# Kernel optimization log

Hardware: AMD Instinct MI355X
Metric: run time of the kernel (lower is better)

The kernel has to match this reference:

```python
import jax, jax.numpy as jnp
import numpy as np

ROPE_THETA = 10000.0
NUM_HEADS = 16


def apply_rope(x, pos, theta=ROPE_THETA):
    # x: [b, h, s, d_h]; pos: [s] int positions
    d = x.shape[-1]
    inv_freq = 1.0 / (theta ** (jnp.arange(0, d, 2, dtype=jnp.float32) / d))  # [d/2]
    ang = pos.astype(jnp.float32)[:, None] * inv_freq[None, :]  # [s, d/2]
    cos, sin = jnp.cos(ang), jnp.sin(ang)
    x1, x2 = x[..., 0::2], x[..., 1::2]  # interleaved pairs
    r1 = x1 * cos - x2 * sin
    r2 = x1 * sin + x2 * cos
    return jnp.stack([r1, r2], axis=-1).reshape(x.shape)


def setup_inputs() -> dict:
    key = jax.random.key(0)
    k1, k2, k3 = jax.random.split(key, 3)
    B, S, D = 4, 2048, 1024
    x = jax.random.normal(k1, (B, S, D), dtype=jnp.float32)
    W_qkv = jax.random.normal(k2, (3, D, D), dtype=jnp.float32) * 0.02
    W_o = jax.random.normal(k3, (D, D), dtype=jnp.float32) * 0.02
    token_positions = jnp.arange(S, dtype=jnp.int32)
    return {"x": x, "W_qkv": W_qkv, "W_o": W_o, "token_positions": token_positions}


def reference(x, W_qkv, W_o, token_positions):
    B, S, D = x.shape
    H = NUM_HEADS
    dh = D // H
    # fused QKV projection: [3, b, s, d]
    qkv = jnp.einsum('bsd,kod->kbso', x, W_qkv)
    # split heads: [3, b, h, s, d_h]
    qkv = qkv.reshape(3, B, S, H, dh).transpose(0, 1, 3, 2, 4)
    q, k, v = qkv[0], qkv[1], qkv[2]
    q = apply_rope(q, token_positions)
    k = apply_rope(k, token_positions)
    scores = jnp.einsum('bhqd,bhkd->bhqk', q, k) / jnp.sqrt(jnp.float32(dh))
    causal = jnp.tril(jnp.ones((S, S), dtype=bool))
    scores = jnp.where(causal, scores, jnp.finfo(scores.dtype).min)
    probs = jax.nn.softmax(scores, axis=-1)
    out = jnp.einsum('bhqk,bhkd->bhqd', probs, v)
    out = out.transpose(0, 2, 1, 3).reshape(B, S, D)  # merge heads
    return out @ W_o.T
```

## Files before the change

### kernel.cpp

```cpp
#include <hip/hip_runtime.h>

typedef unsigned short ushort_t;
typedef unsigned int uint_t;
typedef __bf16 bf16_t;
typedef bf16_t bf16x8 __attribute__((ext_vector_type(8)));
typedef float floatx4 __attribute__((ext_vector_type(4)));

typedef const __attribute__((address_space(1))) uint_t* gptr_t;
typedef __attribute__((address_space(3))) uint_t* lptr_t;

#define BATCH 4
#define SEQ   2048
#define DMODEL 1024
#define NHEAD 16
#define DH    64
#define BHSD  (BATCH*NHEAD*SEQ*DH)
#define QSCALE 0.18033688f
#define MFIX2  11.5415603f

#define NX4 (BATCH*SEQ*DMODEL/4)
#define NW4 (3*DMODEL*DMODEL/4)
#define NO4 (DMODEL*DMODEL/4)
#define NTB (SEQ*32)
#define NSETUP (NX4+NW4+NO4+NTB)

__device__ __forceinline__ float b2f(ushort_t u) {
    uint_t x = ((uint_t)u) << 16;
    return __uint_as_float(x);
}
__device__ __forceinline__ ushort_t f2b(float f) {
    uint_t u = __float_as_uint(f);
    u = (u + 0x7fffu + ((u >> 16) & 1u)) >> 16;
    return (ushort_t)u;
}

__global__ __launch_bounds__(256) void setup_kernel(
    const float* __restrict__ x_f, const float* __restrict__ wq_f,
    const float* __restrict__ wo_f, const int* __restrict__ tp,
    ushort_t* __restrict__ xb, ushort_t* __restrict__ wqb,
    ushort_t* __restrict__ wob, float* __restrict__ ct,
    float* __restrict__ st)
{
    int idx = blockIdx.x * 256 + threadIdx.x;
    if (idx < NX4) {
        float4 v = *(const float4*)&x_f[idx * 4];
        ushort4 o;
        o.x = f2b(v.x); o.y = f2b(v.y); o.z = f2b(v.z); o.w = f2b(v.w);
        *(ushort4*)&xb[idx * 4] = o;
    } else if (idx < NX4 + NW4) {
        int i = idx - NX4;
        float4 v = *(const float4*)&wq_f[i * 4];
        ushort4 o;
        o.x = f2b(v.x); o.y = f2b(v.y); o.z = f2b(v.z); o.w = f2b(v.w);
        *(ushort4*)&wqb[i * 4] = o;
    } else if (idx < NX4 + NW4 + NO4) {
        int i = idx - (NX4 + NW4);
        float4 v = *(const float4*)&wo_f[i * 4];
        ushort4 o;
        o.x = f2b(v.x); o.y = f2b(v.y); o.z = f2b(v.z); o.w = f2b(v.w);
        *(ushort4*)&wob[i * 4] = o;
    } else {
        int i = idx - (NX4 + NW4 + NO4);
        int s = i >> 5;
        int fi = i & 31;
        float pos = (float)tp[s];
        float invf = expf(-(float)fi * 0.28782313662425572f);
        float sv, cv;
        sincosf(pos * invf, &sv, &cv);
        ct[i] = cv;
        st[i] = sv;
    }
}

__device__ __forceinline__ void gemm_bt_tile(
    const ushort_t* __restrict__ A, const ushort_t* __restrict__ B, int K,
    int mbase, int nbase, floatx4 acc[4][4],
    ushort_t* __restrict__ As, ushort_t* __restrict__ Bs)
{
    const int tid  = threadIdx.x;
    const int lane = tid & 63;
    const int wave = tid >> 6;
    const int wm   = (wave >> 1) << 6;
    const int wn   = (wave & 1) << 6;
    const int quad = lane >> 4;
    const int l16  = lane & 15;
    const int lrow = lane >> 3;
    const int lcol = (((lane & 7) ^ lrow) << 3);
    const int rsw  = l16 & 7;

#pragma unroll
    for (int mi = 0; mi < 4; mi++)
#pragma unroll
        for (int ni = 0; ni < 4; ni++)
            acc[mi][ni] = (floatx4){0.f, 0.f, 0.f, 0.f};

    for (int k0 = 0; k0 < K; k0 += 64) {
        __syncthreads();
#pragma unroll
        for (int c = 0; c < 4; ++c) {
            int chunk = wave * 4 + c;
            int row = chunk * 8 + lrow;
            __builtin_amdgcn_global_load_lds(
                (gptr_t)&A[(size_t)(mbase + row) * K + k0 + lcol],
                (lptr_t)&As[chunk * 512], 16, 0, 0);
            __builtin_amdgcn_global_load_lds(
                (gptr_t)&B[(size_t)(nbase + row) * K + k0 + lcol],
                (lptr_t)&Bs[chunk * 512], 16, 0, 0);
        }
        __syncthreads();

#pragma unroll
        for (int kq = 0; kq < 2; ++kq) {
            const int cg = ((kq * 4 + quad) ^ rsw) * 8;
            bf16x8 af[4], bfr[4];
#pragma unroll
            for (int i = 0; i < 4; i++)
                af[i]  = *(const bf16x8*)&As[(wm + i * 16 + l16) * 64 + cg];
#pragma unroll
            for (int i = 0; i < 4; i++)
                bfr[i] = *(const bf16x8*)&Bs[(wn + i * 16 + l16) * 64 + cg];

#pragma unroll
            for (int mi = 0; mi < 4; mi++)
#pragma unroll
                for (int ni = 0; ni < 4; ni++)
                    acc[mi][ni] = __builtin_amdgcn_mfma_f32_16x16x32_bf16(
                        af[mi], bfr[ni], acc[mi][ni], 0, 0, 0);
        }
    }
}

__global__ __launch_bounds__(256) void qkv_rope_kernel(
    const ushort_t* __restrict__ x, const ushort_t* __restrict__ Wqkv,
    const float* __restrict__ ctab, const float* __restrict__ stab,
    ushort_t* __restrict__ qkv)
{
    __shared__ __align__(16) ushort_t As[128 * 64];
    __shared__ __align__(16) ushort_t Bs[128 * 64];
    __shared__ __align__(16) ushort_t T[32 * 136];
    floatx4 acc[4][4];

    const int which = blockIdx.z;
    const int mbase = blockIdx.x * 128;
    const int nbase = blockIdx.y * 128;

    gemm_bt_tile(x, Wqkv + (size_t)which * DMODEL * DMODEL, DMODEL,
                 mbase, nbase, acc, As, Bs);

    const int tid  = threadIdx.x;
    const int lane = tid & 63;
    const int wave = tid >> 6;
    const int wm = (wave >> 1) << 6, wn = (wave & 1) << 6;
    const int quad = lane >> 4, l16 = lane & 15;
    const int wrow0 = (wm ? 16 : 0) + quad * 4;

    for (int mi = 0; mi < 4; mi++) {
#pragma unroll
        for (int ni = 0; ni < 4; ni++) {
#pragma unroll
            for (int r = 0; r < 4; r++) {
                int grow = mbase + wm + mi * 16 + quad * 4 + r;
                int gcol = nbase + wn + ni * 16 + l16;
                float val = acc[mi][ni][r];
                float partner = __shfl_xor(val, 1);
                int s  = grow & (SEQ - 1);
                int dd = gcol & (DH - 1);
                float res = val;
                if (which < 2) {
                    int fi = dd >> 1;
                    float cs = ctab[s * 32 + fi];
                    float sn = stab[s * 32 + fi];
                    res = (gcol & 1) ? fmaf(partner, sn, val * cs)
                                     : fmaf(val, cs, -partner * sn);
                }
                if (which == 0) res *= QSCALE;
                T[(wrow0 + r) * 136 + wn + ni * 16 + l16] = f2b(res);
            }
        }
        __syncthreads();

#pragma unroll
        for (int cc = 0; cc < 2; ++cc) {
            int c = cc * 256 + tid;
            int q2 = c >> 7, ci = c & 127;
            int rgrp = q2 >> 1, hh = q2 & 1;
            int growb = mbase + rgrp * 64;
            int bb = growb >> 11;
            int hidx = (nbase >> 6) + hh;
            size_t bufb = ((size_t)bb * NHEAD + hidx) * ((size_t)SEQ * DH);
            if (which == 0) {
                int row16 = ci >> 3, dd8 = (ci & 7) << 3;
                int s = (growb & (SEQ - 1)) + mi * 16 + row16;
                uint4 d = *(const uint4*)&T[(rgrp * 16 + row16) * 136 + hh * 64 + dd8];
                *(uint4*)&qkv[bufb + (size_t)s * DH + dd8] = d;
            } else {
                int kt = (growb & (SEQ - 1)) >> 6;
                if (which == 1) {
                    int kc = ci >> 6, rem = ci & 63;
                    int qd = rem >> 4, lk = rem & 15;
                    int cflat = (kc * 4 + mi) * 64 + qd * 16 + lk;
                    uint4 d = *(const uint4*)&T[(rgrp * 16 + lk) * 136 + hh * 64 + kc * 32 + qd * 8];
                    *(uint4*)&qkv[(size_t)BHSD + bufb + (size_t)kt * 4096 + cflat * 8] = d;
                } else {
                    int tt = ci >> 6, rem = ci & 63;
                    int nd = rem >> 4, lv = rem & 15;
                    int cflat = ((mi >> 1) * 4 + nd) * 64 + ((mi * 2 + tt) & 3) * 16 + lv;
                    ushort_t tmp[8];
#pragma unroll
                    for (int j = 0; j < 8; ++j)
                        tmp[j] = T[(rgrp * 16 + tt * 8 + j) * 136 + hh * 64 + nd * 16 + lv];
                    *(uint4*)&qkv[2 * (size_t)BHSD + bufb + (size_t)kt * 4096 + cflat * 8]
                        = *(uint4*)tmp;
                }
            }
        }
        __syncthreads();
    }
}

__global__ __launch_bounds__(64) void attn_mfma_kernel(
    const ushort_t* __restrict__ q, const ushort_t* __restrict__ kf,
    const ushort_t* __restrict__ vf, ushort_t* __restrict__ attnout)
{
    __shared__ __align__(16) ushort_t Pw[32 * 72];

    const int lane = threadIdx.x;
    const int quad = lane >> 4;
    const int l16  = lane & 15;
    const int bid = blockIdx.x;
    const int bh = (bid & 7) * 8 + ((bid >> 3) & 7);
    const int chunk = 63 - (bid >> 6);
    const int b = bh >> 4, h = bh & 15;
    const size_t base = (size_t)bh * SEQ * DH;
    const int q0w = chunk * 32;

    bf16x8 qf[2][2];
#pragma unroll
    for (int mi = 0; mi < 2; mi++)
#pragma unroll
        for (int kc = 0; kc < 2; kc++)
            qf[mi][kc] = *(const bf16x8*)&q[base
                + (size_t)(q0w + mi * 16 + l16) * DH + kc * 32 + quad * 8];

    floatx4 o[2][4];
    float lp[2][4];
#pragma unroll
    for (int mi = 0; mi < 2; mi++)
#pragma unroll
        for (int nd = 0; nd < 4; nd++)
            o[mi][nd] = (floatx4){0.f, 0.f, 0.f, 0.f};
#pragma unroll
    for (int mi = 0; mi < 2; mi++)
#pragma unroll
        for (int r = 0; r < 4; r++)
            lp[mi][r] = 0.f;

    const int ktmax = (q0w + 31) >> 6;

    for (int kt = 0; kt <= ktmax; ++kt) {
        const ushort_t* ktb = &kf[base + (size_t)kt * 4096];
        const ushort_t* vtb = &vf[base + (size_t)kt * 4096];

        floatx4 s[2][4];
#pragma unroll
        for (int mi = 0; mi < 2; mi++)
#pragma unroll
            for (int ni = 0; ni < 4; ni++)
                s[mi][ni] = (floatx4){0.f, 0.f, 0.f, 0.f};
#pragma unroll
        for (int kc = 0; kc < 2; kc++) {
            bf16x8 kfr[4];
#pragma unroll
            for (int ni = 0; ni < 4; ni++)
                kfr[ni] = *(const bf16x8*)&ktb[(kc * 4 + ni) * 512 + lane * 8];
#pragma unroll
            for (int mi = 0; mi < 2; mi++)
#pragma unroll
                for (int ni = 0; ni < 4; ni++)
                    s[mi][ni] = __builtin_amdgcn_mfma_f32_16x16x32_bf16(
                        qf[mi][kc], kfr[ni], s[mi][ni], 0, 0, 0);
        }

        bf16x8 vfr[2][4];
#pragma unroll
        for (int kc = 0; kc < 2; kc++)
#pragma unroll
            for (int nd = 0; nd < 4; nd++)
                vfr[kc][nd] = *(const bf16x8*)&vtb[(kc * 4 + nd) * 512 + lane * 8];

        const bool needs_mask = (kt == ktmax);

#pragma unroll
        for (int mi = 0; mi < 2; mi++) {
#pragma unroll
            for (int r = 0; r < 4; r++) {
                if (needs_mask) {
                    int row_g = q0w + mi * 16 + quad * 4 + r;
#pragma unroll
                    for (int ni = 0; ni < 4; ni++) {
                        int col_g = kt * 64 + ni * 16 + l16;
                        s[mi][ni][r] = (col_g <= row_g) ? s[mi][ni][r]
                                                        : -INFINITY;
                    }
                }
                float acc = 0.f;
#pragma unroll
                for (int ni = 0; ni < 4; ni++) {
                    float p = exp2f(s[mi][ni][r] - MFIX2);
                    s[mi][ni][r] = p;
                    acc += p;
                }
                lp[mi][r] += acc;
            }
        }

#pragma unroll
        for (int mi = 0; mi < 2; mi++)
#pragma unroll
            for (int ni = 0; ni < 4; ni++)
#pragma unroll
                for (int r = 0; r < 4; r++)
                    Pw[(mi * 16 + quad * 4 + r) * 72 + ni * 16 + l16]
                        = f2b(s[mi][ni][r]);

#pragma unroll
        for (int kc = 0; kc < 2; kc++) {
            bf16x8 pf[2];
#pragma unroll
            for (int mi = 0; mi < 2; mi++)
                pf[mi] = *(const bf16x8*)&Pw[(mi * 16 + l16) * 72 + kc * 32 + quad * 8];
#pragma unroll
            for (int mi = 0; mi < 2; mi++)
#pragma unroll
                for (int nd = 0; nd < 4; nd++)
                    o[mi][nd] = __builtin_amdgcn_mfma_f32_16x16x32_bf16(
                        pf[mi], vfr[kc][nd], o[mi][nd], 0, 0, 0);
        }
    }

#pragma unroll
    for (int mi = 0; mi < 2; mi++)
#pragma unroll
        for (int r = 0; r < 4; r++) {
            float lf = lp[mi][r];
            lf += __shfl_xor(lf, 1);
            lf += __shfl_xor(lf, 2);
            lf += __shfl_xor(lf, 4);
            lf += __shfl_xor(lf, 8);
            lp[mi][r] = 1.0f / lf;
        }
#pragma unroll
    for (int mi = 0; mi < 2; mi++)
#pragma unroll
        for (int nd = 0; nd < 4; nd++)
#pragma unroll
            for (int r = 0; r < 4; r++) {
                int s_idx = q0w + mi * 16 + quad * 4 + r;
                float val = o[mi][nd][r] * lp[mi][r];
                attnout[((size_t)(b * SEQ + s_idx)) * DMODEL + h * DH + nd * 16 + l16]
                    = f2b(val);
            }
}

__global__ __launch_bounds__(256) void outproj_kernel(
    const ushort_t* __restrict__ Ain, const ushort_t* __restrict__ Wo,
    float* __restrict__ out)
{
    __shared__ __align__(16) ushort_t As[128 * 64];
    __shared__ __align__(16) ushort_t Bs[128 * 64];
    floatx4 acc[4][4];

    const int mbase = blockIdx.x * 128;
    const int nbase = blockIdx.y * 128;
    gemm_bt_tile(Ain, Wo, DMODEL, mbase, nbase, acc, As, Bs);

    const int lane = threadIdx.x & 63;
    const int wave = threadIdx.x >> 6;
    const int wm = (wave >> 1) << 6, wn = (wave & 1) << 6;
    const int quad = lane >> 4, l16 = lane & 15;

#pragma unroll
    for (int mi = 0; mi < 4; mi++)
#pragma unroll
        for (int ni = 0; ni < 4; ni++)
#pragma unroll
            for (int r = 0; r < 4; r++) {
                int grow = mbase + wm + mi * 16 + quad * 4 + r;
                int gcol = nbase + wn + ni * 16 + l16;
                out[(size_t)grow * DMODEL + gcol] = acc[mi][ni][r];
            }
}

extern "C" void kernel_launch(void* const* d_in, const int* in_sizes, int n_in,
                              void* d_out, int out_size, void* d_ws, size_t ws_size,
                              hipStream_t stream) {
    const float* x_f    = (const float*)d_in[0];
    const float* Wqkv_f = (const float*)d_in[1];
    const float* Wo_f   = (const float*)d_in[2];
    const int* tp       = (const int*)d_in[3];
    float* out          = (float*)d_out;

    char* ws = (char*)d_ws;
    ushort_t* qkv     = (ushort_t*)(ws);
    ushort_t* attnout = (ushort_t*)(ws + 50331648);
    float* ctab       = (float*)(ws + 67108864);
    float* stab       = (float*)(ws + 67371008);
    ushort_t* xb      = (ushort_t*)(ws + 67633152);
    ushort_t* Wqkvb   = (ushort_t*)(ws + 84410368);
    ushort_t* Wob     = (ushort_t*)(ws + 90701824);

    setup_kernel<<<dim3(NSETUP / 256), dim3(256), 0, stream>>>(
        x_f, Wqkv_f, Wo_f, tp, xb, Wqkvb, Wob, ctab, stab);

    qkv_rope_kernel<<<dim3(BATCH * SEQ / 128, DMODEL / 128, 3), dim3(256), 0, stream>>>(
        xb, Wqkvb, ctab, stab, qkv);

    attn_mfma_kernel<<<dim3(4096), dim3(64), 0, stream>>>(
        qkv, qkv + (size_t)BHSD, qkv + 2 * (size_t)BHSD, attnout);

    outproj_kernel<<<dim3(BATCH * SEQ / 128, DMODEL / 128), dim3(256), 0, stream>>>(
        attnout, Wob, out);
}
```

Baseline: 280.7 us.

## Process 64 query rows per attention wave to reuse K/V tiles

```diff
diff --git a/kernel.cpp b/kernel.cpp
--- a/kernel.cpp
+++ b/kernel.cpp
@@ -222,64 +222,49 @@
     const ushort_t* __restrict__ q, const ushort_t* __restrict__ kf,
     const ushort_t* __restrict__ vf, ushort_t* __restrict__ attnout)
 {
-    __shared__ __align__(16) ushort_t Pw[32 * 72];
+    __shared__ __align__(16) ushort_t Pw[64 * 72];
 
     const int lane = threadIdx.x;
     const int quad = lane >> 4;
     const int l16  = lane & 15;
     const int bid = blockIdx.x;
     const int bh = (bid & 7) * 8 + ((bid >> 3) & 7);
-    const int chunk = 63 - (bid >> 6);
+    const int g  = 31 - (bid >> 6);
     const int b = bh >> 4, h = bh & 15;
     const size_t base = (size_t)bh * SEQ * DH;
-    const int q0w = chunk * 32;
-
-    bf16x8 qf[2][2];
-#pragma unroll
-    for (int mi = 0; mi < 2; mi++)
+    const int q0w = g * 64;
+
+    bf16x8 qf[4][2];
+#pragma unroll
+    for (int mi = 0; mi < 4; mi++)
 #pragma unroll
         for (int kc = 0; kc < 2; kc++)
             qf[mi][kc] = *(const bf16x8*)&q[base
                 + (size_t)(q0w + mi * 16 + l16) * DH + kc * 32 + quad * 8];
 
-    floatx4 o[2][4];
-    float lp[2][4];
-#pragma unroll
-    for (int mi = 0; mi < 2; mi++)
+    floatx4 o[4][4];
+    float lp[4][4];
+#pragma unroll
+    for (int mi = 0; mi < 4; mi++)
 #pragma unroll
         for (int nd = 0; nd < 4; nd++)
             o[mi][nd] = (floatx4){0.f, 0.f, 0.f, 0.f};
 #pragma unroll
-    for (int mi = 0; mi < 2; mi++)
+    for (int mi = 0; mi < 4; mi++)
 #pragma unroll
         for (int r = 0; r < 4; r++)
             lp[mi][r] = 0.f;
 
-    const int ktmax = (q0w + 31) >> 6;
-
-    for (int kt = 0; kt <= ktmax; ++kt) {
+    for (int kt = 0; kt <= g; ++kt) {
         const ushort_t* ktb = &kf[base + (size_t)kt * 4096];
         const ushort_t* vtb = &vf[base + (size_t)kt * 4096];
 
-        floatx4 s[2][4];
-#pragma unroll
-        for (int mi = 0; mi < 2; mi++)
+        bf16x8 kfr[2][4];
+#pragma unroll
+        for (int kc = 0; kc < 2; kc++)
 #pragma unroll
             for (int ni = 0; ni < 4; ni++)
-                s[mi][ni] = (floatx4){0.f, 0.f, 0.f, 0.f};
-#pragma unroll
-        for (int kc = 0; kc < 2; kc++) {
-            bf16x8 kfr[4];
-#pragma unroll
-            for (int ni = 0; ni < 4; ni++)
-                kfr[ni] = *(const bf16x8*)&ktb[(kc * 4 + ni) * 512 + lane * 8];
-#pragma unroll
-            for (int mi = 0; mi < 2; mi++)
-#pragma unroll
-                for (int ni = 0; ni < 4; ni++)
-                    s[mi][ni] = __builtin_amdgcn_mfma_f32_16x16x32_bf16(
-                        qf[mi][kc], kfr[ni], s[mi][ni], 0, 0, 0);
-        }
+                kfr[kc][ni] = *(const bf16x8*)&ktb[(kc * 4 + ni) * 512 + lane * 8];
 
         bf16x8 vfr[2][4];
 #pragma unroll
@@ -288,49 +273,67 @@
             for (int nd = 0; nd < 4; nd++)
                 vfr[kc][nd] = *(const bf16x8*)&vtb[(kc * 4 + nd) * 512 + lane * 8];
 
-        const bool needs_mask = (kt == ktmax);
-
-#pragma unroll
-        for (int mi = 0; mi < 2; mi++) {
-#pragma unroll
-            for (int r = 0; r < 4; r++) {
-                if (needs_mask) {
-                    int row_g = q0w + mi * 16 + quad * 4 + r;
+        const bool needs_mask = (kt == g);
+
+#pragma unroll
+        for (int hh = 0; hh < 2; ++hh) {
+            floatx4 s[2][4];
+#pragma unroll
+            for (int m2 = 0; m2 < 2; m2++)
+#pragma unroll
+                for (int ni = 0; ni < 4; ni++)
+                    s[m2][ni] = (floatx4){0.f, 0.f, 0.f, 0.f};
+#pragma unroll
+            for (int kc = 0; kc < 2; kc++)
+#pragma unroll
+                for (int m2 = 0; m2 < 2; m2++)
+#pragma unroll
+                    for (int ni = 0; ni < 4; ni++)
+                        s[m2][ni] = __builtin_amdgcn_mfma_f32_16x16x32_bf16(
+                            qf[hh * 2 + m2][kc], kfr[kc][ni], s[m2][ni], 0, 0, 0);
+
+#pragma unroll
+            for (int m2 = 0; m2 < 2; m2++) {
+#pragma unroll
+                for (int r = 0; r < 4; r++) {
+                    if (needs_mask) {
+                        int row_g = q0w + (hh * 2 + m2) * 16 + quad * 4 + r;
+#pragma unroll
+                        for (int ni = 0; ni < 4; ni++) {
+                            int col_g = q0w + ni * 16 + l16;
+                            s[m2][ni][r] = (col_g <= row_g) ? s[m2][ni][r]
+                                                            : -INFINITY;
+                        }
+                    }
+                    float accv = 0.f;
 #pragma unroll
                     for (int ni = 0; ni < 4; ni++) {
-                        int col_g = kt * 64 + ni * 16 + l16;
-                        s[mi][ni][r] = (col_g <= row_g) ? s[mi][ni][r]
-                                                        : -INFINITY;
+                        float p = exp2f(s[m2][ni][r] - MFIX2);
+                        s[m2][ni][r] = p;
+                        accv += p;
                     }
+                    lp[hh * 2 + m2][r] += accv;
                 }
-                float acc = 0.f;
-#pragma unroll
-                for (int ni = 0; ni < 4; ni++) {
-                    float p = exp2f(s[mi][ni][r] - MFIX2);
-                    s[mi][ni][r] = p;
-                    acc += p;
-                }
-                lp[mi][r] += acc;
             }
-        }
-
-#pragma unroll
-        for (int mi = 0; mi < 2; mi++)
-#pragma unroll
-            for (int ni = 0; ni < 4; ni++)
-#pragma unroll
-                for (int r = 0; r < 4; r++)
-                    Pw[(mi * 16 + quad * 4 + r) * 72 + ni * 16 + l16]
-                        = f2b(s[mi][ni][r]);
+
+#pragma unroll
+            for (int m2 = 0; m2 < 2; m2++)
+#pragma unroll
+                for (int ni = 0; ni < 4; ni++)
+#pragma unroll
+                    for (int r = 0; r < 4; r++)
+                        Pw[((hh * 2 + m2) * 16 + quad * 4 + r) * 72 + ni * 16 + l16]
+                            = f2b(s[m2][ni][r]);
+        }
 
 #pragma unroll
         for (int kc = 0; kc < 2; kc++) {
-            bf16x8 pf[2];
-#pragma unroll
-            for (int mi = 0; mi < 2; mi++)
+            bf16x8 pf[4];
+#pragma unroll
+            for (int mi = 0; mi < 4; mi++)
                 pf[mi] = *(const bf16x8*)&Pw[(mi * 16 + l16) * 72 + kc * 32 + quad * 8];
 #pragma unroll
-            for (int mi = 0; mi < 2; mi++)
+            for (int mi = 0; mi < 4; mi++)
 #pragma unroll
                 for (int nd = 0; nd < 4; nd++)
                     o[mi][nd] = __builtin_amdgcn_mfma_f32_16x16x32_bf16(
@@ -339,7 +342,7 @@
     }
 
 #pragma unroll
-    for (int mi = 0; mi < 2; mi++)
+    for (int mi = 0; mi < 4; mi++)
 #pragma unroll
         for (int r = 0; r < 4; r++) {
             float lf = lp[mi][r];
@@ -350,7 +353,7 @@
             lp[mi][r] = 1.0f / lf;
         }
 #pragma unroll
-    for (int mi = 0; mi < 2; mi++)
+    for (int mi = 0; mi < 4; mi++)
 #pragma unroll
         for (int nd = 0; nd < 4; nd++)
 #pragma unroll
@@ -415,7 +418,7 @@
     qkv_rope_kernel<<<dim3(BATCH * SEQ / 128, DMODEL / 128, 3), dim3(256), 0, stream>>>(
         xb, Wqkvb, ctab, stab, qkv);
 
-    attn_mfma_kernel<<<dim3(4096), dim3(64), 0, stream>>>(
+    attn_mfma_kernel<<<dim3(2048), dim3(64), 0, stream>>>(
         qkv, qkv + (size_t)BHSD, qkv + 2 * (size_t)BHSD, attnout);
 
     outproj_kernel<<<dim3(BATCH * SEQ / 128, DMODEL / 128), dim3(256), 0, stream>>>(
```

New measurement: 296.2 us. 5.5% more time.
